# Performance work log

Measured on AMD Instinct MI355X. Metric: run time of the kernel, lower is better.

The kernel has to match this reference:

```python
import jax, jax.numpy as jnp
import numpy as np

N, E = 50000, 600000
NODE_DIM, EDGE_DIM, MSG_DIM = 128, 64, 128


def setup_inputs() -> dict:
    key = jax.random.key(0)
    ks = jax.random.split(key, 8)
    s = 0.05
    return {
        "node_features": jax.random.normal(ks[0], (N, NODE_DIM), jnp.float32),
        "edge_features": jax.random.normal(ks[1], (E, EDGE_DIM), jnp.float32),
        "edge_index": jax.random.randint(ks[2], (2, E), 0, N, jnp.int32),
        "We1": jax.random.normal(ks[3], (2 * NODE_DIM + EDGE_DIM, 32), jnp.float32) * s,
        "be1": jnp.zeros((32,), jnp.float32),
        "We2": jax.random.normal(ks[4], (32, MSG_DIM), jnp.float32) * s,
        "be2": jnp.zeros((MSG_DIM,), jnp.float32),
        "Wn1": jax.random.normal(ks[5], (NODE_DIM + MSG_DIM, 64), jnp.float32) * s,
        "bn1": jnp.zeros((64,), jnp.float32),
        "Wn2": jax.random.normal(ks[6], (64, MSG_DIM), jnp.float32) * s,
        "bn2": jnp.zeros((MSG_DIM,), jnp.float32),
    }


def reference(node_features, edge_features, edge_index,
              We1, be1, We2, be2, Wn1, bn1, Wn2, bn2):
    src, dst = edge_index[0], edge_index[1]
    src_f = node_features[src]            # [E, node_dim] gather
    dst_f = node_features[dst]            # [E, node_dim] gather
    # edge message encoder: 2-layer MLP with ReLU
    edge_in = jnp.concatenate([src_f, dst_f, edge_features], axis=1)  # [E, 2*nd+ed]
    h = jax.nn.relu(edge_in @ We1 + be1)
    edge_msg = jax.nn.relu(h @ We2 + be2)  # [E, msg_dim]
    # node message encoder
    node_in = jnp.concatenate([dst_f, edge_msg], axis=1)  # [E, nd+md]
    h2 = jax.nn.relu(node_in @ Wn1 + bn1)
    node_msg = jax.nn.relu(h2 @ Wn2 + bn2)  # [E, msg_dim]
    # scatter-sum over destination nodes (replaces the O(N) python loop)
    agg = jax.ops.segment_sum(node_msg, dst, num_segments=node_features.shape[0])
    return node_features + agg
```

## Files before the change

kernel.cpp:

```cpp
#include <hip/hip_runtime.h>
#include <hip/hip_bf16.h>

constexpr int N_NODES = 50000;
constexpr int N_EDGES = 600000;
constexpr int ND = 128;
constexpr int ED = 64;
constexpr int MD = 128;
constexpr int H1 = 32;
constexpr int H2 = 64;

typedef __attribute__((ext_vector_type(8))) short short8;
typedef __attribute__((ext_vector_type(4))) float f32x4;
typedef __attribute__((ext_vector_type(4))) unsigned int uint32x4;

#define MFMA16(a, b, c) __builtin_amdgcn_mfma_f32_16x16x32_bf16((a), (b), (c), 0, 0, 0)

constexpr int COUNTS_PAD = 53248;
constexpr size_t WS_MSGS    = 0;
constexpr size_t WS_PRE     = WS_MSGS + (size_t)N_EDGES * MD * 2;
constexpr size_t WS_POS     = WS_PRE + (size_t)N_NODES * 128 * 2;
constexpr size_t WS_COUNTS  = WS_POS + (size_t)N_EDGES * 4;
constexpr size_t WS_OFFSETS = WS_COUNTS + (size_t)COUNTS_PAD * 4;
constexpr size_t WS_WFE     = ((WS_OFFSETS + (size_t)(N_NODES + 1) * 4 + 15) / 16) * 16;
constexpr size_t WS_WFN     = WS_WFE + (size_t)44 * 64 * 16;
constexpr size_t WS_END     = WS_WFN + (size_t)32 * 64 * 16;

__device__ inline float bflo(unsigned u) { return __uint_as_float(u << 16); }
__device__ inline float bfhi(unsigned u) { return __uint_as_float(u & 0xffff0000u); }
__device__ inline short f2bf(float f) {
    __hip_bfloat16 h = __float2bfloat16(f);
    return *reinterpret_cast<short*>(&h);
}
__device__ inline unsigned pkbf(float a, float b) {
    unsigned r;
    asm("v_cvt_pk_bf16_f32 %0, %1, %2" : "=v"(r) : "v"(a), "v"(b));
    return r;
}
__device__ inline unsigned prelu(float a, float b) {
    return pkbf(fmaxf(a, 0.0f), fmaxf(b, 0.0f));
}
__device__ inline short8 pack8(unsigned w0, unsigned w1, unsigned w2, unsigned w3) {
    uint32x4 t{w0, w1, w2, w3};
    return __builtin_bit_cast(short8, t);
}

__device__ inline int hperm(int kt, int kq) {
    return (kt * 2 + ((kq >> 2) & 1)) * 16 + ((kq >> 3) & 3) * 4 + (kq & 3);
}

__global__ __launch_bounds__(256) void wprep(
    const float* __restrict__ We1, const float* __restrict__ We2,
    const float* __restrict__ Wn1, const float* __restrict__ Wn2,
    short8* __restrict__ wfE, short8* __restrict__ wfN)
{
    const int g = blockIdx.x * 256 + threadIdx.x;
    const int lane = g & 63;
    const int f = g >> 6;
    const int m16 = lane & 15, quad = lane >> 4;
    short v[8];
    if (f < 44) {
        #pragma unroll
        for (int j = 0; j < 8; ++j) {
            const int kq = quad * 8 + j;
            float s;
            if (f < 4) {
                const int kt = f >> 1, mt = f & 1;
                s = We1[(size_t)(2 * ND + kt * 32 + kq) * H1 + mt * 16 + m16];
            } else if (f < 12) {
                const int mt = f - 4;
                s = We2[(size_t)hperm(0, kq) * MD + mt * 16 + m16];
            } else if (f < 28) {
                const int ff = f - 12, kt = ff >> 2, mt = ff & 3;
                s = Wn1[(size_t)(ND + hperm(kt, kq)) * H2 + mt * 16 + m16];
            } else {
                const int ff = f - 28, kt = ff >> 3, mt = ff & 7;
                s = Wn2[(size_t)hperm(kt, kq) * MD + mt * 16 + m16];
            }
            v[j] = f2bf(s);
        }
        wfE[g] = short8{v[0], v[1], v[2], v[3], v[4], v[5], v[6], v[7]};
    } else {
        const int ff = f - 44, kt = ff >> 3, nt = ff & 7;
        const int n = nt * 16 + m16;
        #pragma unroll
        for (int j = 0; j < 8; ++j) {
            const int k = kt * 32 + quad * 8 + j;
            float s;
            if (n < 32)      s = We1[(size_t)k * H1 + n];
            else if (n < 64) s = We1[(size_t)(ND + k) * H1 + (n - 32)];
            else             s = Wn1[(size_t)k * H2 + (n - 64)];
            v[j] = f2bf(s);
        }
        wfN[(size_t)(f - 44) * 64 + lane] = short8{v[0], v[1], v[2], v[3], v[4], v[5], v[6], v[7]};
    }
}

__global__ __launch_bounds__(256) void hist_pos(const int* __restrict__ eidx,
                                                int* __restrict__ counts,
                                                int* __restrict__ pos) {
    const int e = blockIdx.x * 256 + threadIdx.x;
    if (e < N_EDGES) pos[e] = atomicAdd(&counts[eidx[N_EDGES + e]], 1);
}

__global__ __launch_bounds__(1024) void scan_kernel(const int* __restrict__ counts,
                                                    int* __restrict__ offsets) {
    constexpr int T = 1024;
    constexpr int CHUNK = 52;
    const int tid = threadIdx.x;
    const int base = tid * CHUNK;
    int4 v[13];
    int s = 0;
    const int4* pc = (const int4*)(counts + base);
    #pragma unroll
    for (int i = 0; i < 13; ++i) {
        v[i] = pc[i];
        s += v[i].x + v[i].y + v[i].z + v[i].w;
    }
    __shared__ int sm[T];
    sm[tid] = s;
    __syncthreads();
    for (int off = 1; off < T; off <<= 1) {
        const int t = (tid >= off) ? sm[tid - off] : 0;
        __syncthreads();
        sm[tid] += t;
        __syncthreads();
    }
    int run = sm[tid] - s;
    #pragma unroll
    for (int i = 0; i < 13; ++i) {
        const int idx = base + i * 4;
        if (idx     <= N_NODES) offsets[idx]     = run;  run += v[i].x;
        if (idx + 1 <= N_NODES) offsets[idx + 1] = run;  run += v[i].y;
        if (idx + 2 <= N_NODES) offsets[idx + 2] = run;  run += v[i].z;
        if (idx + 3 <= N_NODES) offsets[idx + 3] = run;  run += v[i].w;
    }
}

__global__ __launch_bounds__(256) void node_pre_mfma(
    const float* __restrict__ nf, const short8* __restrict__ wfN,
    unsigned short* __restrict__ pre)
{
    __shared__ short ost[4][2048];
    const int tid = threadIdx.x;
    const int w = tid >> 6, lane = tid & 63;
    const int m16 = lane & 15, quad = lane >> 4;
    const int n0 = blockIdx.x * 64 + w * 16;

    short8 a[4];
    #pragma unroll
    for (int kt = 0; kt < 4; ++kt) {
        const int node = min(n0 + m16, N_NODES - 1);
        const float* pn = nf + (size_t)node * ND + kt * 32 + quad * 8;
        const float4 f0 = *(const float4*)pn;
        const float4 f1 = *(const float4*)(pn + 4);
        a[kt] = pack8(pkbf(f0.x, f0.y), pkbf(f0.z, f0.w),
                      pkbf(f1.x, f1.y), pkbf(f1.z, f1.w));
    }
    f32x4 acc[8];
    #pragma unroll
    for (int nt = 0; nt < 8; ++nt) acc[nt] = f32x4{0.f, 0.f, 0.f, 0.f};
    #pragma unroll
    for (int kt = 0; kt < 4; ++kt) {
        #pragma unroll
        for (int nt = 0; nt < 8; ++nt)
            acc[nt] = MFMA16(a[kt], wfN[(size_t)(kt * 8 + nt) * 64 + lane], acc[nt]);
    }
    short* o = &ost[w][0];
    #pragma unroll
    for (int nt = 0; nt < 8; ++nt)
        #pragma unroll
        for (int r = 0; r < 4; ++r)
            o[(quad * 4 + r) * 128 + nt * 16 + m16] = f2bf(acc[nt][r]);
    asm volatile("s_waitcnt lgkmcnt(0)" ::: "memory");
    #pragma unroll
    for (int i = 0; i < 4; ++i) {
        const int row = i * 4 + quad;
        const int node = n0 + row;
        if (node < N_NODES) {
            const uint4 v = ((const uint4*)(o + row * 128))[m16];
            *((uint4*)(pre + (size_t)node * 128) + m16) = v;
        }
    }
}

__global__ __launch_bounds__(256, 5) void edge_mfma(
    const float* __restrict__ ef, const int* __restrict__ eidx,
    const unsigned short* __restrict__ pre,
    const int* __restrict__ pos, const int* __restrict__ offsets,
    const short8* __restrict__ wfE,
    const float* __restrict__ be1, const float* __restrict__ be2,
    const float* __restrict__ bn1, const float* __restrict__ bn2,
    unsigned short* __restrict__ msgs)
{
    constexpr int TE = 64;
    __shared__ __align__(16) char sws[4][4608];
    __shared__ int slotlds[TE];

    const int tid = threadIdx.x;
    const int e0 = blockIdx.x * TE;
    const int w = tid >> 6, lane = tid & 63;
    const int m16 = lane & 15, q = lane >> 4;
    const int er0 = w * 16;
    char* swsb = &sws[w][0];

    float4 efv0, efv1, efv2, efv3;
    {
        const float* pe = ef + (size_t)(e0 + er0 + m16) * ED + q * 8;
        efv0 = *(const float4*)pe;
        efv1 = *(const float4*)(pe + 4);
        efv2 = *(const float4*)(pe + 32);
        efv3 = *(const float4*)(pe + 36);
    }

    {
        const int et = tid >> 2, p = tid & 3;
        const int e = e0 + et;
        const int src = eidx[e];
        const int dst = eidx[N_EDGES + e];
        const uint4* pa = (const uint4*)(pre + (size_t)src * 128);
        const uint4* pd = (const uint4*)(pre + (size_t)dst * 128);
        const uint4 ua = pa[p];
        const uint4 ud = pd[4 + p];
        const uint4 s0 = pd[8 + 2 * p];
        const uint4 s1 = pd[9 + 2 * p];
        const float4 b0 = ((const float4*)be1)[2 * p];
        const float4 b1 = ((const float4*)be1)[2 * p + 1];
        float4 r0, r1;
        r0.x = bflo(ua.x) + bflo(ud.x) + b0.x;
        r0.y = bfhi(ua.x) + bfhi(ud.x) + b0.y;
        r0.z = bflo(ua.y) + bflo(ud.y) + b0.z;
        r0.w = bfhi(ua.y) + bfhi(ud.y) + b0.w;
        r1.x = bflo(ua.z) + bflo(ud.z) + b1.x;
        r1.y = bfhi(ua.z) + bfhi(ud.z) + b1.y;
        r1.z = bflo(ua.w) + bflo(ud.w) + b1.z;
        r1.w = bfhi(ua.w) + bfhi(ud.w) + b1.w;
        char* wb = &sws[et >> 4][0] + (et & 15) * 144;
        *(float4*)(wb + p * 32) = r0;
        *(float4*)(wb + p * 32 + 16) = r1;
        char* wb2 = &sws[et >> 4][2304] + (et & 15) * 144;
        *(uint4*)(wb2 + p * 32) = s0;
        *(uint4*)(wb2 + p * 32 + 16) = s1;
        if (p == 3) slotlds[et] = offsets[dst] + pos[e];
    }
    asm volatile("s_waitcnt lgkmcnt(0)" ::: "memory");

    const short8 aef0 = pack8(pkbf(efv0.x, efv0.y), pkbf(efv0.z, efv0.w),
                              pkbf(efv1.x, efv1.y), pkbf(efv1.z, efv1.w));
    const short8 aef1 = pack8(pkbf(efv2.x, efv2.y), pkbf(efv2.z, efv2.w),
                              pkbf(efv3.x, efv3.y), pkbf(efv3.z, efv3.w));

    f32x4 acc1[2];
    #pragma unroll
    for (int mt = 0; mt < 2; ++mt)
        acc1[mt] = *(const f32x4*)(swsb + m16 * 144 + mt * 64 + q * 16);
    #pragma unroll
    for (int mt = 0; mt < 2; ++mt) {
        acc1[mt] = MFMA16(wfE[(size_t)(0 + mt) * 64 + lane], aef0, acc1[mt]);
        acc1[mt] = MFMA16(wfE[(size_t)(2 + mt) * 64 + lane], aef1, acc1[mt]);
    }

    const short8 b2 = pack8(prelu(acc1[0][0], acc1[0][1]), prelu(acc1[0][2], acc1[0][3]),
                            prelu(acc1[1][0], acc1[1][1]), prelu(acc1[1][2], acc1[1][3]));

    f32x4 acc2[8];
    #pragma unroll
    for (int mt = 0; mt < 8; ++mt) {
        const float4 bb = *(const float4*)(be2 + mt * 16 + q * 4);
        acc2[mt] = f32x4{bb.x, bb.y, bb.z, bb.w};
        acc2[mt] = MFMA16(wfE[(size_t)(4 + mt) * 64 + lane], b2, acc2[mt]);
    }
    short8 b3[4];
    #pragma unroll
    for (int kt = 0; kt < 4; ++kt)
        b3[kt] = pack8(prelu(acc2[2 * kt][0], acc2[2 * kt][1]),
                       prelu(acc2[2 * kt][2], acc2[2 * kt][3]),
                       prelu(acc2[2 * kt + 1][0], acc2[2 * kt + 1][1]),
                       prelu(acc2[2 * kt + 1][2], acc2[2 * kt + 1][3]));

    f32x4 acc3[4];
    #pragma unroll
    for (int mt = 0; mt < 4; ++mt) {
        const float4 bb = *(const float4*)(bn1 + mt * 16 + q * 4);
        const uint2 ua = *(const uint2*)(swsb + 2304 + m16 * 144 + mt * 32 + q * 8);
        acc3[mt] = f32x4{bb.x + bflo(ua.x), bb.y + bfhi(ua.x),
                         bb.z + bflo(ua.y), bb.w + bfhi(ua.y)};
    }
    #pragma unroll
    for (int kt = 0; kt < 4; ++kt) {
        #pragma unroll
        for (int mt = 0; mt < 4; ++mt)
            acc3[mt] = MFMA16(wfE[(size_t)(12 + kt * 4 + mt) * 64 + lane], b3[kt], acc3[mt]);
    }
    short8 b4[2];
    #pragma unroll
    for (int kt = 0; kt < 2; ++kt)
        b4[kt] = pack8(prelu(acc3[2 * kt][0], acc3[2 * kt][1]),
                       prelu(acc3[2 * kt][2], acc3[2 * kt][3]),
                       prelu(acc3[2 * kt + 1][0], acc3[2 * kt + 1][1]),
                       prelu(acc3[2 * kt + 1][2], acc3[2 * kt + 1][3]));

    f32x4 acc4[8];
    #pragma unroll
    for (int mt = 0; mt < 8; ++mt) {
        const float4 bb = *(const float4*)(bn2 + mt * 16 + q * 4);
        acc4[mt] = f32x4{bb.x, bb.y, bb.z, bb.w};
    }
    #pragma unroll
    for (int kt = 0; kt < 2; ++kt) {
        #pragma unroll
        for (int mt = 0; mt < 8; ++mt)
            acc4[mt] = MFMA16(wfE[(size_t)(28 + kt * 8 + mt) * 64 + lane], b4[kt], acc4[mt]);
    }

    #pragma unroll
    for (int mt = 0; mt < 8; ++mt) {
        uint2 wv;
        wv.x = prelu(acc4[mt][0], acc4[mt][1]);
        wv.y = prelu(acc4[mt][2], acc4[mt][3]);
        *(uint2*)(swsb + m16 * 272 + mt * 32 + q * 8) = wv;
    }
    asm volatile("s_waitcnt lgkmcnt(0)" ::: "memory");

    #pragma unroll
    for (int i = 0; i < 4; ++i) {
        const int row = i * 4 + q;
        const int sl = slotlds[er0 + row];
        const uint4 v = *(const uint4*)(swsb + row * 272 + m16 * 16);
        *((uint4*)(msgs + (size_t)sl * 128) + m16) = v;
    }
}

__global__ __launch_bounds__(256) void gather2(
    const float* __restrict__ nf,
    const uint4* __restrict__ msgs4,
    const int* __restrict__ offsets,
    float* __restrict__ out)
{
    const int node = blockIdx.x * 16 + (threadIdx.x >> 4);
    const int m16 = threadIdx.x & 15;

    const float4* pn = (const float4*)(nf + (size_t)node * ND) + m16 * 2;
    const float4 n0 = pn[0];
    const float4 n1 = pn[1];

    const int beg = offsets[node];
    const int end = offsets[node + 1];

    float4 s0 = float4{0.f, 0.f, 0.f, 0.f};
    float4 s1 = float4{0.f, 0.f, 0.f, 0.f};
    const uint4* p = msgs4 + (size_t)beg * 16 + m16;
    int i = beg;
    for (; i + 1 < end; i += 2, p += 32) {
        const uint4 u0 = p[0];
        const uint4 u1 = p[16];
        s0.x += bflo(u0.x); s0.y += bfhi(u0.x);
        s0.z += bflo(u0.y); s0.w += bfhi(u0.y);
        s1.x += bflo(u0.z); s1.y += bfhi(u0.z);
        s1.z += bflo(u0.w); s1.w += bfhi(u0.w);
        s0.x += bflo(u1.x); s0.y += bfhi(u1.x);
        s0.z += bflo(u1.y); s0.w += bfhi(u1.y);
        s1.x += bflo(u1.z); s1.y += bfhi(u1.z);
        s1.z += bflo(u1.w); s1.w += bfhi(u1.w);
    }
    if (i < end) {
        const uint4 u = p[0];
        s0.x += bflo(u.x); s0.y += bfhi(u.x);
        s0.z += bflo(u.y); s0.w += bfhi(u.y);
        s1.x += bflo(u.z); s1.y += bfhi(u.z);
        s1.z += bflo(u.w); s1.w += bfhi(u.w);
    }
    s0.x += n0.x; s0.y += n0.y; s0.z += n0.z; s0.w += n0.w;
    s1.x += n1.x; s1.y += n1.y; s1.z += n1.z; s1.w += n1.w;

    float4* po = (float4*)(out + (size_t)node * ND) + m16 * 2;
    po[0] = s0;
    po[1] = s1;
}

extern "C" void kernel_launch(void* const* d_in, const int* in_sizes, int n_in,
                              void* d_out, int out_size, void* d_ws, size_t ws_size,
                              hipStream_t stream) {
    const float* nf  = (const float*)d_in[0];
    const float* ef  = (const float*)d_in[1];
    const int*  eidx = (const int*)d_in[2];
    const float* We1 = (const float*)d_in[3];
    const float* be1 = (const float*)d_in[4];
    const float* We2 = (const float*)d_in[5];
    const float* be2 = (const float*)d_in[6];
    const float* Wn1 = (const float*)d_in[7];
    const float* bn1 = (const float*)d_in[8];
    const float* Wn2 = (const float*)d_in[9];
    const float* bn2 = (const float*)d_in[10];
    float* out = (float*)d_out;

    char* ws = (char*)d_ws;
    unsigned short* msgs = (unsigned short*)(ws + WS_MSGS);
    unsigned short* pre  = (unsigned short*)(ws + WS_PRE);
    int* pos             = (int*)(ws + WS_POS);
    int* counts          = (int*)(ws + WS_COUNTS);
    int* offsets         = (int*)(ws + WS_OFFSETS);
    short8* wfE          = (short8*)(ws + WS_WFE);
    short8* wfN          = (short8*)(ws + WS_WFN);
    (void)ws_size; (void)WS_END;

    hipMemsetAsync(counts, 0, (size_t)COUNTS_PAD * 4, stream);
    wprep<<<19, 256, 0, stream>>>(We1, We2, Wn1, Wn2, wfE, wfN);
    hist_pos<<<(N_EDGES + 255) / 256, 256, 0, stream>>>(eidx, counts, pos);
    scan_kernel<<<1, 1024, 0, stream>>>(counts, offsets);
    node_pre_mfma<<<(N_NODES + 63) / 64, 256, 0, stream>>>(nf, wfN, pre);
    edge_mfma<<<N_EDGES / 64, 256, 0, stream>>>(
        ef, eidx, pre, pos, offsets, wfE, be1, be2, bn1, bn2, msgs);
    gather2<<<N_NODES / 16, 256, 0, stream>>>(nf, (const uint4*)msgs, offsets, out);
}
```

Measured before the change: 459.2 us.

## Process two 64-edge tiles per edge_mfma block and unroll gather by four

The edge kernel now handles 128 edges per block as two interleaved 64-edge tiles. Each MFMA weight fragment loaded from global memory is reused for both tiles, and the doubled independent MFMA chains give more latency hiding. The cost is more registers and twice the LDS per block, so occupancy is lowered to 4 waves per SIMD. The gather kernel is unrolled to four messages per iteration with two accumulator sets to raise memory-level parallelism.

```diff
diff --git a/kernel.cpp b/kernel.cpp
--- a/kernel.cpp
+++ b/kernel.cpp
@@ -105,9 +105,8 @@
 __global__ __launch_bounds__(1024) void scan_kernel(const int* __restrict__ counts,
                                                     int* __restrict__ offsets) {
     constexpr int T = 1024;
-    constexpr int CHUNK = 52;
     const int tid = threadIdx.x;
-    const int base = tid * CHUNK;
+    const int base = tid * 52;
     int4 v[13];
     int s = 0;
     const int4* pc = (const int4*)(counts + base);
@@ -183,7 +182,7 @@
     }
 }
 
-__global__ __launch_bounds__(256, 5) void edge_mfma(
+__global__ __launch_bounds__(256, 4) void edge_mfma(
     const float* __restrict__ ef, const int* __restrict__ eidx,
     const unsigned short* __restrict__ pre,
     const int* __restrict__ pos, const int* __restrict__ offsets,
@@ -192,141 +191,221 @@
     const float* __restrict__ bn1, const float* __restrict__ bn2,
     unsigned short* __restrict__ msgs)
 {
-    constexpr int TE = 64;
-    __shared__ __align__(16) char sws[4][4608];
+    constexpr int TE = 128;
+    __shared__ __align__(16) char sws[4][9216];
     __shared__ int slotlds[TE];
 
     const int tid = threadIdx.x;
     const int e0 = blockIdx.x * TE;
+    const bool hasB = (e0 + 64) < N_EDGES;
     const int w = tid >> 6, lane = tid & 63;
     const int m16 = lane & 15, q = lane >> 4;
     const int er0 = w * 16;
     char* swsb = &sws[w][0];
 
-    float4 efv0, efv1, efv2, efv3;
+    float4 efv[2][4];
     {
         const float* pe = ef + (size_t)(e0 + er0 + m16) * ED + q * 8;
-        efv0 = *(const float4*)pe;
-        efv1 = *(const float4*)(pe + 4);
-        efv2 = *(const float4*)(pe + 32);
-        efv3 = *(const float4*)(pe + 36);
+        efv[0][0] = *(const float4*)pe;
+        efv[0][1] = *(const float4*)(pe + 4);
+        efv[0][2] = *(const float4*)(pe + 32);
+        efv[0][3] = *(const float4*)(pe + 36);
+        if (hasB) {
+            const float* pe2 = pe + (size_t)64 * ED;
+            efv[1][0] = *(const float4*)pe2;
+            efv[1][1] = *(const float4*)(pe2 + 4);
+            efv[1][2] = *(const float4*)(pe2 + 32);
+            efv[1][3] = *(const float4*)(pe2 + 36);
+        }
     }
 
     {
-        const int et = tid >> 2, p = tid & 3;
-        const int e = e0 + et;
-        const int src = eidx[e];
-        const int dst = eidx[N_EDGES + e];
-        const uint4* pa = (const uint4*)(pre + (size_t)src * 128);
-        const uint4* pd = (const uint4*)(pre + (size_t)dst * 128);
-        const uint4 ua = pa[p];
-        const uint4 ud = pd[4 + p];
-        const uint4 s0 = pd[8 + 2 * p];
-        const uint4 s1 = pd[9 + 2 * p];
-        const float4 b0 = ((const float4*)be1)[2 * p];
-        const float4 b1 = ((const float4*)be1)[2 * p + 1];
-        float4 r0, r1;
-        r0.x = bflo(ua.x) + bflo(ud.x) + b0.x;
-        r0.y = bfhi(ua.x) + bfhi(ud.x) + b0.y;
-        r0.z = bflo(ua.y) + bflo(ud.y) + b0.z;
-        r0.w = bfhi(ua.y) + bfhi(ud.y) + b0.w;
-        r1.x = bflo(ua.z) + bflo(ud.z) + b1.x;
-        r1.y = bfhi(ua.z) + bfhi(ud.z) + b1.y;
-        r1.z = bflo(ua.w) + bflo(ud.w) + b1.z;
-        r1.w = bfhi(ua.w) + bfhi(ud.w) + b1.w;
-        char* wb = &sws[et >> 4][0] + (et & 15) * 144;
-        *(float4*)(wb + p * 32) = r0;
-        *(float4*)(wb + p * 32 + 16) = r1;
-        char* wb2 = &sws[et >> 4][2304] + (et & 15) * 144;
-        *(uint4*)(wb2 + p * 32) = s0;
-        *(uint4*)(wb2 + p * 32 + 16) = s1;
-        if (p == 3) slotlds[et] = offsets[dst] + pos[e];
+        const int et = tid >> 2, p4 = tid & 3;
+        const int eA = e0 + et;
+        const int srcA = eidx[eA];
+        const int dstA = eidx[N_EDGES + eA];
+        const uint4* paA = (const uint4*)(pre + (size_t)srcA * 128);
+        const uint4* pdA = (const uint4*)(pre + (size_t)dstA * 128);
+        const uint4 uaA = paA[p4];
+        const uint4 udA = pdA[4 + p4];
+        const uint4 s0A = pdA[8 + 2 * p4];
+        const uint4 s1A = pdA[9 + 2 * p4];
+        const int slA = offsets[dstA] + pos[eA];
+
+        uint4 uaB, udB, s0B, s1B;
+        int slB = 0;
+        if (hasB) {
+            const int eB = eA + 64;
+            const int srcB = eidx[eB];
+            const int dstB = eidx[N_EDGES + eB];
+            const uint4* paB = (const uint4*)(pre + (size_t)srcB * 128);
+            const uint4* pdB = (const uint4*)(pre + (size_t)dstB * 128);
+            uaB = paB[p4];
+            udB = pdB[4 + p4];
+            s0B = pdB[8 + 2 * p4];
+            s1B = pdB[9 + 2 * p4];
+            slB = offsets[dstB] + pos[eB];
+        }
+        const float4 b0 = ((const float4*)be1)[2 * p4];
+        const float4 b1 = ((const float4*)be1)[2 * p4 + 1];
+
+        char* wbase = &sws[et >> 4][0] + (et & 15) * 144;
+        {
+            float4 r0, r1;
+            r0.x = bflo(uaA.x) + bflo(udA.x) + b0.x;
+            r0.y = bfhi(uaA.x) + bfhi(udA.x) + b0.y;
+            r0.z = bflo(uaA.y) + bflo(udA.y) + b0.z;
+            r0.w = bfhi(uaA.y) + bfhi(udA.y) + b0.w;
+            r1.x = bflo(uaA.z) + bflo(udA.z) + b1.x;
+            r1.y = bfhi(uaA.z) + bfhi(udA.z) + b1.y;
+            r1.z = bflo(uaA.w) + bflo(udA.w) + b1.z;
+            r1.w = bfhi(uaA.w) + bfhi(udA.w) + b1.w;
+            *(float4*)(wbase + p4 * 32) = r0;
+            *(float4*)(wbase + p4 * 32 + 16) = r1;
+            *(uint4*)(wbase + 2304 + p4 * 32) = s0A;
+            *(uint4*)(wbase + 2304 + p4 * 32 + 16) = s1A;
+            if (p4 == 3) slotlds[et] = slA;
+        }
+        if (hasB) {
+            float4 r0, r1;
+            r0.x = bflo(uaB.x) + bflo(udB.x) + b0.x;
+            r0.y = bfhi(uaB.x) + bfhi(udB.x) + b0.y;
+            r0.z = bflo(uaB.y) + bflo(udB.y) + b0.z;
+            r0.w = bfhi(uaB.y) + bfhi(udB.y) + b0.w;
+            r1.x = bflo(uaB.z) + bflo(udB.z) + b1.x;
+            r1.y = bfhi(uaB.z) + bfhi(udB.z) + b1.y;
+            r1.z = bflo(uaB.w) + bflo(udB.w) + b1.z;
+            r1.w = bfhi(uaB.w) + bfhi(udB.w) + b1.w;
+            *(float4*)(wbase + 4608 + p4 * 32) = r0;
+            *(float4*)(wbase + 4608 + p4 * 32 + 16) = r1;
+            *(uint4*)(wbase + 4608 + 2304 + p4 * 32) = s0B;
+            *(uint4*)(wbase + 4608 + 2304 + p4 * 32 + 16) = s1B;
+            if (p4 == 3) slotlds[64 + et] = slB;
+        }
     }
     asm volatile("s_waitcnt lgkmcnt(0)" ::: "memory");
 
-    const short8 aef0 = pack8(pkbf(efv0.x, efv0.y), pkbf(efv0.z, efv0.w),
-                              pkbf(efv1.x, efv1.y), pkbf(efv1.z, efv1.w));
-    const short8 aef1 = pack8(pkbf(efv2.x, efv2.y), pkbf(efv2.z, efv2.w),
-                              pkbf(efv3.x, efv3.y), pkbf(efv3.z, efv3.w));
-
-    f32x4 acc1[2];
-    #pragma unroll
-    for (int mt = 0; mt < 2; ++mt)
-        acc1[mt] = *(const f32x4*)(swsb + m16 * 144 + mt * 64 + q * 16);
-    #pragma unroll
-    for (int mt = 0; mt < 2; ++mt) {
-        acc1[mt] = MFMA16(wfE[(size_t)(0 + mt) * 64 + lane], aef0, acc1[mt]);
-        acc1[mt] = MFMA16(wfE[(size_t)(2 + mt) * 64 + lane], aef1, acc1[mt]);
-    }
-
-    const short8 b2 = pack8(prelu(acc1[0][0], acc1[0][1]), prelu(acc1[0][2], acc1[0][3]),
-                            prelu(acc1[1][0], acc1[1][1]), prelu(acc1[1][2], acc1[1][3]));
-
-    f32x4 acc2[8];
+    short8 aef[2][2];
+    #pragma unroll
+    for (int t = 0; t < 2; ++t) {
+        aef[t][0] = pack8(pkbf(efv[t][0].x, efv[t][0].y), pkbf(efv[t][0].z, efv[t][0].w),
+                          pkbf(efv[t][1].x, efv[t][1].y), pkbf(efv[t][1].z, efv[t][1].w));
+        aef[t][1] = pack8(pkbf(efv[t][2].x, efv[t][2].y), pkbf(efv[t][2].z, efv[t][2].w),
+                          pkbf(efv[t][3].x, efv[t][3].y), pkbf(efv[t][3].z, efv[t][3].w));
+    }
+
+    f32x4 acc1[2][2];
+    #pragma unroll
+    for (int t = 0; t < 2; ++t)
+        #pragma unroll
+        for (int mt = 0; mt < 2; ++mt)
+            acc1[t][mt] = *(const f32x4*)(swsb + t * 4608 + m16 * 144 + mt * 64 + q * 16);
+    #pragma unroll
+    for (int kt = 0; kt < 2; ++kt)
+        #pragma unroll
+        for (int mt = 0; mt < 2; ++mt) {
+            const short8 wf = wfE[(size_t)(kt * 2 + mt) * 64 + lane];
+            acc1[0][mt] = MFMA16(wf, aef[0][kt], acc1[0][mt]);
+            acc1[1][mt] = MFMA16(wf, aef[1][kt], acc1[1][mt]);
+        }
+
+    short8 b2[2];
+    #pragma unroll
+    for (int t = 0; t < 2; ++t)
+        b2[t] = pack8(prelu(acc1[t][0][0], acc1[t][0][1]), prelu(acc1[t][0][2], acc1[t][0][3]),
+                      prelu(acc1[t][1][0], acc1[t][1][1]), prelu(acc1[t][1][2], acc1[t][1][3]));
+
+    f32x4 acc2[2][8];
     #pragma unroll
     for (int mt = 0; mt < 8; ++mt) {
         const float4 bb = *(const float4*)(be2 + mt * 16 + q * 4);
-        acc2[mt] = f32x4{bb.x, bb.y, bb.z, bb.w};
-        acc2[mt] = MFMA16(wfE[(size_t)(4 + mt) * 64 + lane], b2, acc2[mt]);
-    }
-    short8 b3[4];
-    #pragma unroll
-    for (int kt = 0; kt < 4; ++kt)
-        b3[kt] = pack8(prelu(acc2[2 * kt][0], acc2[2 * kt][1]),
-                       prelu(acc2[2 * kt][2], acc2[2 * kt][3]),
-                       prelu(acc2[2 * kt + 1][0], acc2[2 * kt + 1][1]),
-                       prelu(acc2[2 * kt + 1][2], acc2[2 * kt + 1][3]));
-
-    f32x4 acc3[4];
+        const short8 wf = wfE[(size_t)(4 + mt) * 64 + lane];
+        acc2[0][mt] = f32x4{bb.x, bb.y, bb.z, bb.w};
+        acc2[1][mt] = acc2[0][mt];
+        acc2[0][mt] = MFMA16(wf, b2[0], acc2[0][mt]);
+        acc2[1][mt] = MFMA16(wf, b2[1], acc2[1][mt]);
+    }
+    short8 b3[2][4];
+    #pragma unroll
+    for (int t = 0; t < 2; ++t)
+        #pragma unroll
+        for (int kt = 0; kt < 4; ++kt)
+            b3[t][kt] = pack8(prelu(acc2[t][2 * kt][0], acc2[t][2 * kt][1]),
+                              prelu(acc2[t][2 * kt][2], acc2[t][2 * kt][3]),
+                              prelu(acc2[t][2 * kt + 1][0], acc2[t][2 * kt + 1][1]),
+                              prelu(acc2[t][2 * kt + 1][2], acc2[t][2 * kt + 1][3]));
+
+    f32x4 acc3[2][4];
     #pragma unroll
     for (int mt = 0; mt < 4; ++mt) {
         const float4 bb = *(const float4*)(bn1 + mt * 16 + q * 4);
-        const uint2 ua = *(const uint2*)(swsb + 2304 + m16 * 144 + mt * 32 + q * 8);
-        acc3[mt] = f32x4{bb.x + bflo(ua.x), bb.y + bfhi(ua.x),
-                         bb.z + bflo(ua.y), bb.w + bfhi(ua.y)};
-    }
-    #pragma unroll
-    for (int kt = 0; kt < 4; ++kt) {
-        #pragma unroll
-        for (int mt = 0; mt < 4; ++mt)
-            acc3[mt] = MFMA16(wfE[(size_t)(12 + kt * 4 + mt) * 64 + lane], b3[kt], acc3[mt]);
-    }
-    short8 b4[2];
-    #pragma unroll
-    for (int kt = 0; kt < 2; ++kt)
-        b4[kt] = pack8(prelu(acc3[2 * kt][0], acc3[2 * kt][1]),
-                       prelu(acc3[2 * kt][2], acc3[2 * kt][3]),
-                       prelu(acc3[2 * kt + 1][0], acc3[2 * kt + 1][1]),
-                       prelu(acc3[2 * kt + 1][2], acc3[2 * kt + 1][3]));
-
-    f32x4 acc4[8];
+        #pragma unroll
+        for (int t = 0; t < 2; ++t) {
+            const uint2 ua = *(const uint2*)(swsb + t * 4608 + 2304 + m16 * 144 + mt * 32 + q * 8);
+            acc3[t][mt] = f32x4{bb.x + bflo(ua.x), bb.y + bfhi(ua.x),
+                                bb.z + bflo(ua.y), bb.w + bfhi(ua.y)};
+        }
+    }
+    #pragma unroll
+    for (int kt = 0; kt < 4; ++kt)
+        #pragma unroll
+        for (int mt = 0; mt < 4; ++mt) {
+            const short8 wf = wfE[(size_t)(12 + kt * 4 + mt) * 64 + lane];
+            acc3[0][mt] = MFMA16(wf, b3[0][kt], acc3[0][mt]);
+            acc3[1][mt] = MFMA16(wf, b3[1][kt], acc3[1][mt]);
+        }
+    short8 b4[2][2];
+    #pragma unroll
+    for (int t = 0; t < 2; ++t)
+        #pragma unroll
+        for (int kt = 0; kt < 2; ++kt)
+            b4[t][kt] = pack8(prelu(acc3[t][2 * kt][0], acc3[t][2 * kt][1]),
+                              prelu(acc3[t][2 * kt][2], acc3[t][2 * kt][3]),
+                              prelu(acc3[t][2 * kt + 1][0], acc3[t][2 * kt + 1][1]),
+                              prelu(acc3[t][2 * kt + 1][2], acc3[t][2 * kt + 1][3]));
+
+    f32x4 acc4[2][8];
     #pragma unroll
     for (int mt = 0; mt < 8; ++mt) {
         const float4 bb = *(const float4*)(bn2 + mt * 16 + q * 4);
-        acc4[mt] = f32x4{bb.x, bb.y, bb.z, bb.w};
-    }
-    #pragma unroll
-    for (int kt = 0; kt < 2; ++kt) {
-        #pragma unroll
-        for (int mt = 0; mt < 8; ++mt)
-            acc4[mt] = MFMA16(wfE[(size_t)(28 + kt * 8 + mt) * 64 + lane], b4[kt], acc4[mt]);
-    }
-
-    #pragma unroll
-    for (int mt = 0; mt < 8; ++mt) {
-        uint2 wv;
-        wv.x = prelu(acc4[mt][0], acc4[mt][1]);
-        wv.y = prelu(acc4[mt][2], acc4[mt][3]);
-        *(uint2*)(swsb + m16 * 272 + mt * 32 + q * 8) = wv;
-    }
+        acc4[0][mt] = f32x4{bb.x, bb.y, bb.z, bb.w};
+        acc4[1][mt] = acc4[0][mt];
+    }
+    #pragma unroll
+    for (int kt = 0; kt < 2; ++kt)
+        #pragma unroll
+        for (int mt = 0; mt < 8; ++mt) {
+            const short8 wf = wfE[(size_t)(28 + kt * 8 + mt) * 64 + lane];
+            acc4[0][mt] = MFMA16(wf, b4[0][kt], acc4[0][mt]);
+            acc4[1][mt] = MFMA16(wf, b4[1][kt], acc4[1][mt]);
+        }
+
+    #pragma unroll
+    for (int t = 0; t < 2; ++t)
+        #pragma unroll
+        for (int mt = 0; mt < 8; ++mt) {
+            uint2 wv;
+            wv.x = prelu(acc4[t][mt][0], acc4[t][mt][1]);
+            wv.y = prelu(acc4[t][mt][2], acc4[t][mt][3]);
+            *(uint2*)(swsb + t * 4608 + m16 * 272 + mt * 32 + q * 8) = wv;
+        }
     asm volatile("s_waitcnt lgkmcnt(0)" ::: "memory");
 
     #pragma unroll
     for (int i = 0; i < 4; ++i) {
         const int row = i * 4 + q;
-        const int sl = slotlds[er0 + row];
-        const uint4 v = *(const uint4*)(swsb + row * 272 + m16 * 16);
-        *((uint4*)(msgs + (size_t)sl * 128) + m16) = v;
+        const int slA = slotlds[er0 + row];
+        const uint4 vA = *(const uint4*)(swsb + row * 272 + m16 * 16);
+        *((uint4*)(msgs + (size_t)slA * 128) + m16) = vA;
+    }
+    if (hasB) {
+        #pragma unroll
+        for (int i = 0; i < 4; ++i) {
+            const int row = i * 4 + q;
+            const int slB = slotlds[64 + er0 + row];
+            const uint4 vB = *(const uint4*)(swsb + 4608 + row * 272 + m16 * 16);
+            *((uint4*)(msgs + (size_t)slB * 128) + m16) = vB;
+        }
     }
 }
 
@@ -346,31 +425,34 @@
     const int beg = offsets[node];
     const int end = offsets[node + 1];
 
-    float4 s0 = float4{0.f, 0.f, 0.f, 0.f};
-    float4 s1 = float4{0.f, 0.f, 0.f, 0.f};
+    float4 sA0{0.f, 0.f, 0.f, 0.f}, sA1{0.f, 0.f, 0.f, 0.f};
+    float4 sB0{0.f, 0.f, 0.f, 0.f}, sB1{0.f, 0.f, 0.f, 0.f};
     const uint4* p = msgs4 + (size_t)beg * 16 + m16;
     int i = beg;
-    for (; i + 1 < end; i += 2, p += 32) {
+    for (; i + 3 < end; i += 4, p += 64) {
         const uint4 u0 = p[0];
         const uint4 u1 = p[16];
-        s0.x += bflo(u0.x); s0.y += bfhi(u0.x);
-        s0.z += bflo(u0.y); s0.w += bfhi(u0.y);
-        s1.x += bflo(u0.z); s1.y += bfhi(u0.z);
-        s1.z += bflo(u0.w); s1.w += bfhi(u0.w);
-        s0.x += bflo(u1.x); s0.y += bfhi(u1.x);
-        s0.z += bflo(u1.y); s0.w += bfhi(u1.y);
-        s1.x += bflo(u1.z); s1.y += bfhi(u1.z);
-        s1.z += bflo(u1.w); s1.w += bfhi(u1.w);
-    }
-    if (i < end) {
+        const uint4 u2 = p[32];
+        const uint4 u3 = p[48];
+        sA0.x += bflo(u0.x); sA0.y += bfhi(u0.x); sA0.z += bflo(u0.y); sA0.w += bfhi(u0.y);
+        sA1.x += bflo(u0.z); sA1.y += bfhi(u0.z); sA1.z += bflo(u0.w); sA1.w += bfhi(u0.w);
+        sB0.x += bflo(u1.x); sB0.y += bfhi(u1.x); sB0.z += bflo(u1.y); sB0.w += bfhi(u1.y);
+        sB1.x += bflo(u1.z); sB1.y += bfhi(u1.z); sB1.z += bflo(u1.w); sB1.w += bfhi(u1.w);
+        sA0.x += bflo(u2.x); sA0.y += bfhi(u2.x); sA0.z += bflo(u2.y); sA0.w += bfhi(u2.y);
+        sA1.x += bflo(u2.z); sA1.y += bfhi(u2.z); sA1.z += bflo(u2.w); sA1.w += bfhi(u2.w);
+        sB0.x += bflo(u3.x); sB0.y += bfhi(u3.x); sB0.z += bflo(u3.y); sB0.w += bfhi(u3.y);
+        sB1.x += bflo(u3.z); sB1.y += bfhi(u3.z); sB1.z += bflo(u3.w); sB1.w += bfhi(u3.w);
+    }
+    for (; i < end; ++i, p += 16) {
         const uint4 u = p[0];
-        s0.x += bflo(u.x); s0.y += bfhi(u.x);
-        s0.z += bflo(u.y); s0.w += bfhi(u.y);
-        s1.x += bflo(u.z); s1.y += bfhi(u.z);
-        s1.z += bflo(u.w); s1.w += bfhi(u.w);
-    }
-    s0.x += n0.x; s0.y += n0.y; s0.z += n0.z; s0.w += n0.w;
-    s1.x += n1.x; s1.y += n1.y; s1.z += n1.z; s1.w += n1.w;
+        sA0.x += bflo(u.x); sA0.y += bfhi(u.x); sA0.z += bflo(u.y); sA0.w += bfhi(u.y);
+        sA1.x += bflo(u.z); sA1.y += bfhi(u.z); sA1.z += bflo(u.w); sA1.w += bfhi(u.w);
+    }
+    float4 s0, s1;
+    s0.x = sA0.x + sB0.x + n0.x; s0.y = sA0.y + sB0.y + n0.y;
+    s0.z = sA0.z + sB0.z + n0.z; s0.w = sA0.w + sB0.w + n0.w;
+    s1.x = sA1.x + sB1.x + n1.x; s1.y = sA1.y + sB1.y + n1.y;
+    s1.z = sA1.z + sB1.z + n1.z; s1.w = sA1.w + sB1.w + n1.w;
 
     float4* po = (float4*)(out + (size_t)node * ND) + m16 * 2;
     po[0] = s0;
@@ -408,7 +490,7 @@
     hist_pos<<<(N_EDGES + 255) / 256, 256, 0, stream>>>(eidx, counts, pos);
     scan_kernel<<<1, 1024, 0, stream>>>(counts, offsets);
     node_pre_mfma<<<(N_NODES + 63) / 64, 256, 0, stream>>>(nf, wfN, pre);
-    edge_mfma<<<N_EDGES / 64, 256, 0, stream>>>(
+    edge_mfma<<<(N_EDGES + 127) / 128, 256, 0, stream>>>(
         ef, eidx, pre, pos, offsets, wfE, be1, be2, bn1, bn2, msgs);
     gather2<<<N_NODES / 16, 256, 0, stream>>>(nf, (const uint4*)msgs, offsets, out);
 }
```

Result: faster. 422.6 us (-8.0%).
